# Performance work log

Hardware: AMD Instinct MI355X
Metric: run time of the kernel (lower is better)

## Reference

```python
import jax, jax.numpy as jnp
import numpy as np

PATCH = (160, 160, 160)  # patch_size from init_kwargs


def _zero_centered_mesh(patch):
    # create_zero_centered_coordinate_mesh: meshgrid(range(p), indexing='ij') - (p-1)/2
    axes = [jnp.arange(p, dtype=jnp.float32) - (p - 1) / 2.0 for p in patch]
    return jnp.stack(jnp.meshgrid(*axes, indexing='ij'), axis=0)  # [3, *patch]


def setup_inputs() -> dict:
    key = jax.random.key(0)
    k1, k2 = jax.random.split(key)
    data = jax.random.normal(k1, (4, 2, 192, 192, 192), dtype=jnp.float32)
    seg = jax.random.randint(k2, (4, 2, 192, 192, 192), 0, 4).astype(jnp.float32)
    return {"data": data, "seg": seg}


def reference(data, seg):
    B, C, D, H, W = data.shape
    patch = PATCH
    # zero-centered coordinate mesh, shifted to the center of the input volume
    coords = _zero_centered_mesh(patch)  # [3, pD, pH, pW]
    ctr = jnp.array([(D - 1) / 2.0, (H - 1) / 2.0, (W - 1) / 2.0], dtype=jnp.float32)
    coords = coords + ctr[:, None, None, None]
    coord_list = [coords[0], coords[1], coords[2]]

    # map_coordinates-style resampling of every (b, c) volume at the mesh points
    vols = data.reshape(B * C, D, H, W)
    interp = jax.vmap(
        lambda v: jax.scipy.ndimage.map_coordinates(
            v, coord_list, order=1, mode="constant", cval=0.0
        )
    )
    data_out = interp(vols).reshape(B, C, *patch)

    # center crop of seg (crop_type='center'): lbs = (shape - crop_size) // 2
    lbs = [(s - p) // 2 for s, p in zip((D, H, W), patch)]
    seg_out = seg[
        :,
        :,
        lbs[0] : lbs[0] + patch[0],
        lbs[1] : lbs[1] + patch[1],
        lbs[2] : lbs[2] + patch[2],
    ]
    return data_out, seg_out
```

## Files before the change

### kernel.cpp

```cpp
#include <hip/hip_runtime.h>


constexpr unsigned P    = 160;
constexpr unsigned S    = 192;
constexpr unsigned OFF  = 16;
constexpr unsigned BC   = 8;
constexpr unsigned ROW4 = P / 4;
constexpr unsigned SROW4   = S / 4;
constexpr unsigned SPLANE4 = S * S / 4;
constexpr unsigned SVOL4   = S * S * S / 4;
constexpr unsigned OUT4 = BC * P * P * ROW4;
constexpr unsigned GRID_HALF = OUT4 / 1024;

using f4 = __attribute__((ext_vector_type(4))) float;

__global__ __launch_bounds__(256) void crop_copy_kernel(
    const f4* __restrict__ data,
    const f4* __restrict__ seg,
    f4* __restrict__ out)
{
    const bool is_seg  = blockIdx.x >= GRID_HALF;
    const f4* __restrict__ src_buf = is_seg ? seg : data;
    f4* __restrict__ dst           = out + (is_seg ? OUT4 : 0u);
    const unsigned b  = blockIdx.x - (is_seg ? GRID_HALF : 0u);
    const unsigned o0 = b * 1024u + threadIdx.x;

    unsigned src[4];
#pragma unroll
    for (unsigned k = 0; k < 4; ++k) {
        const unsigned o   = o0 + 256u * k;
        const unsigned w4  = o % ROW4;
        const unsigned row = o / ROW4;
        const unsigned h   = row % P;
        const unsigned t   = row / P;
        const unsigned d   = t % P;
        const unsigned bc  = t / P;
        src[k] = bc * SVOL4 + (d + OFF) * SPLANE4 + (h + OFF) * SROW4
               + (OFF / 4) + w4;
    }

    f4 a0 = __builtin_nontemporal_load(&src_buf[src[0]]);
    f4 a1 = __builtin_nontemporal_load(&src_buf[src[1]]);
    f4 a2 = __builtin_nontemporal_load(&src_buf[src[2]]);
    f4 a3 = __builtin_nontemporal_load(&src_buf[src[3]]);

    dst[o0]        = a0;
    dst[o0 + 256u] = a1;
    dst[o0 + 512u] = a2;
    dst[o0 + 768u] = a3;
}

extern "C" void kernel_launch(void* const* d_in, const int* in_sizes, int n_in,
                              void* d_out, int out_size, void* d_ws, size_t ws_size,
                              hipStream_t stream)
{
    const f4* data = (const f4*)d_in[0];
    const f4* seg  = (const f4*)d_in[1];
    f4* out = (f4*)d_out;

    constexpr unsigned block = 256;
    constexpr unsigned grid  = 2 * GRID_HALF;
    crop_copy_kernel<<<grid, block, 0, stream>>>(data, seg, out);
}
```

Before: 492.1 us.

## Stage contiguous full-width source rows through LDS before writing cropped rows

Result: no change. 485.7 us (-1.3%).

```diff
diff --git a/kernel.cpp b/kernel.cpp
--- a/kernel.cpp
+++ b/kernel.cpp
@@ -10,7 +10,12 @@
 constexpr unsigned SPLANE4 = S * S / 4;
 constexpr unsigned SVOL4   = S * S * S / 4;
 constexpr unsigned OUT4 = BC * P * P * ROW4;
-constexpr unsigned GRID_HALF = OUT4 / 1024;
+
+constexpr unsigned RPB   = 32;
+constexpr unsigned BPP   = P / RPB;
+constexpr unsigned BPT   = BC * P * BPP;
+constexpr unsigned LDSF4 = RPB * SROW4;
+constexpr unsigned OUTF4 = RPB * ROW4;
 
 using f4 = __attribute__((ext_vector_type(4))) float;
 
@@ -19,35 +24,47 @@
     const f4* __restrict__ seg,
     f4* __restrict__ out)
 {
-    const bool is_seg  = blockIdx.x >= GRID_HALF;
+    __shared__ f4 lds[LDSF4];
+
+    const unsigned gb     = blockIdx.x;
+    const bool     is_seg = gb >= BPT;
     const f4* __restrict__ src_buf = is_seg ? seg : data;
-    f4* __restrict__ dst           = out + (is_seg ? OUT4 : 0u);
-    const unsigned b  = blockIdx.x - (is_seg ? GRID_HALF : 0u);
-    const unsigned o0 = b * 1024u + threadIdx.x;
+    const unsigned b  = gb - (is_seg ? BPT : 0u);
+    const unsigned bc = b / (P * BPP);
+    const unsigned r2 = b - bc * (P * BPP);
+    const unsigned d  = r2 / BPP;
+    const unsigned h0 = (r2 - d * BPP) * RPB;
+    const unsigned t  = threadIdx.x;
 
-    unsigned src[4];
+    const unsigned sbase = bc * SVOL4 + (d + OFF) * SPLANE4 + (h0 + OFF) * SROW4;
+
+    f4 v0 = __builtin_nontemporal_load(&src_buf[sbase + t]);
+    f4 v1 = __builtin_nontemporal_load(&src_buf[sbase + t +  256u]);
+    f4 v2 = __builtin_nontemporal_load(&src_buf[sbase + t +  512u]);
+    f4 v3 = __builtin_nontemporal_load(&src_buf[sbase + t +  768u]);
+    f4 v4 = __builtin_nontemporal_load(&src_buf[sbase + t + 1024u]);
+    f4 v5 = __builtin_nontemporal_load(&src_buf[sbase + t + 1280u]);
+
+    lds[t]          = v0;
+    lds[t +  256u]  = v1;
+    lds[t +  512u]  = v2;
+    lds[t +  768u]  = v3;
+    lds[t + 1024u]  = v4;
+    lds[t + 1280u]  = v5;
+
+    __syncthreads();
+
+    const unsigned obase = (is_seg ? OUT4 : 0u)
+                         + ((bc * P + d) * P + h0) * ROW4;
+
 #pragma unroll
-    for (unsigned k = 0; k < 4; ++k) {
-        const unsigned o   = o0 + 256u * k;
-        const unsigned w4  = o % ROW4;
-        const unsigned row = o / ROW4;
-        const unsigned h   = row % P;
-        const unsigned t   = row / P;
-        const unsigned d   = t % P;
-        const unsigned bc  = t / P;
-        src[k] = bc * SVOL4 + (d + OFF) * SPLANE4 + (h + OFF) * SROW4
-               + (OFF / 4) + w4;
+    for (unsigned k = 0; k < 5; ++k) {
+        const unsigned oidx = t + 256u * k;
+        const unsigned r    = oidx / ROW4;
+        const unsigned w    = oidx - r * ROW4;
+        f4 val = lds[r * SROW4 + (OFF / 4) + w];
+        __builtin_nontemporal_store(val, &out[obase + oidx]);
     }
-
-    f4 a0 = __builtin_nontemporal_load(&src_buf[src[0]]);
-    f4 a1 = __builtin_nontemporal_load(&src_buf[src[1]]);
-    f4 a2 = __builtin_nontemporal_load(&src_buf[src[2]]);
-    f4 a3 = __builtin_nontemporal_load(&src_buf[src[3]]);
-
-    dst[o0]        = a0;
-    dst[o0 + 256u] = a1;
-    dst[o0 + 512u] = a2;
-    dst[o0 + 768u] = a3;
 }
 
 extern "C" void kernel_launch(void* const* d_in, const int* in_sizes, int n_in,
@@ -59,6 +76,6 @@
     f4* out = (f4*)d_out;
 
     constexpr unsigned block = 256;
-    constexpr unsigned grid  = 2 * GRID_HALF;
+    constexpr unsigned grid  = 2 * BPT;
     crop_copy_kernel<<<grid, block, 0, stream>>>(data, seg, out);
 }
```
